# Kernel optimization log

Measured on AMD Instinct MI355X. Metric: run time of the kernel, lower is better.

## Reference

```python
import jax, jax.numpy as jnp
import numpy as np

N = 50000          # nodes
E = 800000         # edges (avg degree 16)
D_IN = 128
D_HID = 128
D_OUT = 64
NUM_GRAPHS = 64


def setup_inputs() -> dict:
    key = jax.random.key(0)
    ks = jax.random.split(key, 10)
    x = jax.random.normal(ks[0], (N, D_IN), dtype=jnp.float32)
    edge_index = jax.random.randint(ks[1], (2, E), 0, N, dtype=jnp.int64)
    batch = jnp.sort(jax.random.randint(ks[2], (N,), 0, NUM_GRAPHS, dtype=jnp.int64))
    def glorot(k, fan_in, fan_out):
        s = np.float32(np.sqrt(6.0 / (fan_in + fan_out)))
        return jax.random.uniform(k, (fan_in, fan_out), jnp.float32, -s, s)
    return {
        "x": x,
        "edge_index": edge_index,
        "batch": batch,
        "W1": glorot(ks[3], D_IN, D_HID),  "b1": jnp.zeros((D_HID,), jnp.float32),
        "W2": glorot(ks[4], D_HID, D_HID), "b2": jnp.zeros((D_HID,), jnp.float32),
        "W3": glorot(ks[5], D_HID, D_OUT), "b3": jnp.zeros((D_OUT,), jnp.float32),
    }


def _gcn_conv(x, W, b, src, dst, dis):
    # GCNConv: D^{-1/2}(A+I)D^{-1/2} X W + b  (self-loops handled analytically)
    h = x @ W                                   # [N, out]
    norm = dis[src] * dis[dst]                  # [E]
    agg = jax.ops.segment_sum(h[src] * norm[:, None], dst, num_segments=N)
    return agg + h * (dis * dis)[:, None] + b   # self-loop term + bias


def reference(x, edge_index, batch, W1, b1, W2, b2, W3, b3):
    src, dst = edge_index[0], edge_index[1]
    # degree with self-loop (matches PyG add_self_loops + gcn_norm)
    deg = jnp.zeros((N,), jnp.float32).at[dst].add(1.0) + 1.0
    dis = jax.lax.rsqrt(deg)                    # deg >= 1, no inf handling needed

    h = jax.nn.relu(_gcn_conv(x, W1, b1, src, dst, dis))
    h = jax.nn.relu(_gcn_conv(h, W2, b2, src, dst, dis))
    features = _gcn_conv(h, W3, b3, src, dst, dis)   # [N, D_OUT]

    sums = jax.ops.segment_sum(features, batch, num_segments=NUM_GRAPHS)
    cnts = jax.ops.segment_sum(jnp.ones((N,), jnp.float32), batch, num_segments=NUM_GRAPHS)
    avg_pool = sums / jnp.maximum(cnts, 1.0)[:, None]  # [NUM_GRAPHS, D_OUT]
    return features, avg_pool
```

## Files before the change

kernel.cpp:

```cpp
#include <hip/hip_runtime.h>


constexpr int KDIM = 128;
constexpr int NGRAPH = 64;

__device__ __forceinline__ unsigned bf16rne(float f) {
  unsigned u = __float_as_uint(f);
  return (u + 0x7fffu + ((u >> 16) & 1u)) >> 16;
}
__device__ __forceinline__ unsigned packbf2(float a, float b) {
  return bf16rne(a) | (bf16rne(b) << 16);
}
__device__ __forceinline__ float bflo(unsigned u) {
  return __uint_as_float(u << 16);
}
__device__ __forceinline__ float bfhi(unsigned u) {
  return __uint_as_float(u & 0xffff0000u);
}

__global__ void k_init(int* __restrict__ counts, int n) {
  int i = blockIdx.x * blockDim.x + threadIdx.x;
  int stride = gridDim.x * blockDim.x;
  for (int j = i; j < n; j += stride) counts[j] = 0;
}

__global__ void k_hist(const int* __restrict__ src, const int* __restrict__ dst,
                       int* __restrict__ counts, int e, int n) {
  int i = blockIdx.x * blockDim.x + threadIdx.x;
  int stride = gridDim.x * blockDim.x;
  for (int j = i; j < e; j += stride) {
    int s = src[j], d = dst[j];
    if ((unsigned)s < (unsigned)n && (unsigned)d < (unsigned)n)
      atomicAdd(&counts[d], 1);
  }
}

__global__ void k_dis(const int* __restrict__ counts, float* __restrict__ dis, int n) {
  int i = blockIdx.x * blockDim.x + threadIdx.x;
  int stride = gridDim.x * blockDim.x;
  for (int j = i; j < n; j += stride)
    dis[j] = rsqrtf((float)counts[j] + 1.0f);
}

__global__ void k_scan_block(const int* __restrict__ in, int* __restrict__ outExcl,
                             int* __restrict__ blockSums, int n) {
  __shared__ int s[256];
  int tid = threadIdx.x;
  int i = blockIdx.x * 256 + tid;
  int v = (i < n) ? in[i] : 0;
  int x = v;
  s[tid] = x;
  __syncthreads();
  for (int off = 1; off < 256; off <<= 1) {
    int t = (tid >= off) ? s[tid - off] : 0;
    __syncthreads();
    x += t;
    s[tid] = x;
    __syncthreads();
  }
  if (i < n) outExcl[i] = x - v;
  if (tid == 255) blockSums[blockIdx.x] = x;
}

__global__ void k_scan_offsets(int* __restrict__ bs, int nb) {
  __shared__ int s[256];
  int tid = threadIdx.x;
  int v = (tid < nb) ? bs[tid] : 0;
  int x = v;
  s[tid] = x;
  __syncthreads();
  for (int off = 1; off < 256; off <<= 1) {
    int t = (tid >= off) ? s[tid - off] : 0;
    __syncthreads();
    x += t;
    s[tid] = x;
    __syncthreads();
  }
  if (tid < nb) bs[tid] = x - v;
  if (tid == nb - 1) bs[256] = x;
}

__global__ void k_scan_add(int* __restrict__ row_start, const int* __restrict__ bs,
                           int* __restrict__ cursor, int n) {
  int i = blockIdx.x * blockDim.x + threadIdx.x;
  int stride = gridDim.x * blockDim.x;
  for (int j = i; j < n; j += stride) {
    int r = row_start[j] + bs[j >> 8];
    row_start[j] = r;
    cursor[j] = r;
  }
  if (i == 0) row_start[n] = bs[256];
}

__global__ void k_scatter(const int* __restrict__ src, const int* __restrict__ dst,
                          int* __restrict__ cursor, int* __restrict__ colA,
                          int e, int n) {
  int i = blockIdx.x * blockDim.x + threadIdx.x;
  int stride = gridDim.x * blockDim.x;
  for (int j = i; j < e; j += stride) {
    int s = src[j], d = dst[j];
    if ((unsigned)s < (unsigned)n && (unsigned)d < (unsigned)n) {
      int pos = atomicAdd(&cursor[d], 1);
      colA[pos] = s;
    }
  }
}

template <int DOUT>
__global__ __launch_bounds__(256) void k_gemm2b(const float* __restrict__ X,
                                                const float* __restrict__ W,
                                                unsigned short* __restrict__ Hb,
                                                int n) {
  __shared__ float xT[32][128];
  __shared__ float Wl[32][64];
  const int tid = threadIdx.x;
  const int tr = tid & 15;
  const int tc = tid >> 4;
  const int rowBase = blockIdx.x * 128;
  const int colBase = blockIdx.y * 64;

  float acc[8][4];
#pragma unroll
  for (int i = 0; i < 8; ++i)
#pragma unroll
    for (int j = 0; j < 4; ++j) acc[i][j] = 0.f;

  const int sr = tid >> 1;
  const int kh = (tid & 1) * 16;
  const int srow = min(rowBase + sr, n - 1);
  const float* xsrc = X + (size_t)srow * KDIM + kh;

  for (int k0 = 0; k0 < KDIM / 32; ++k0) {
    {
      const float4* s4 = reinterpret_cast<const float4*>(xsrc + k0 * 32);
      float4 v0 = s4[0], v1 = s4[1], v2 = s4[2], v3 = s4[3];
      xT[kh + 0][sr] = v0.x;  xT[kh + 1][sr] = v0.y;
      xT[kh + 2][sr] = v0.z;  xT[kh + 3][sr] = v0.w;
      xT[kh + 4][sr] = v1.x;  xT[kh + 5][sr] = v1.y;
      xT[kh + 6][sr] = v1.z;  xT[kh + 7][sr] = v1.w;
      xT[kh + 8][sr] = v2.x;  xT[kh + 9][sr] = v2.y;
      xT[kh + 10][sr] = v2.z; xT[kh + 11][sr] = v2.w;
      xT[kh + 12][sr] = v3.x; xT[kh + 13][sr] = v3.y;
      xT[kh + 14][sr] = v3.z; xT[kh + 15][sr] = v3.w;
    }
#pragma unroll
    for (int q = 0; q < 2; ++q) {
      int f4 = tid + q * 256;
      int k = f4 >> 4;
      int c4 = f4 & 15;
      *reinterpret_cast<float4*>(&Wl[k][c4 * 4]) = *reinterpret_cast<const float4*>(
          W + (size_t)(k0 * 32 + k) * DOUT + colBase + c4 * 4);
    }
    __syncthreads();
#pragma unroll 8
    for (int k = 0; k < 32; ++k) {
      float4 xa = *reinterpret_cast<const float4*>(&xT[k][tr * 4]);
      float4 xb = *reinterpret_cast<const float4*>(&xT[k][64 + tr * 4]);
      float4 wv = *reinterpret_cast<const float4*>(&Wl[k][tc * 4]);
      const float xs[8] = {xa.x, xa.y, xa.z, xa.w, xb.x, xb.y, xb.z, xb.w};
      const float ws[4] = {wv.x, wv.y, wv.z, wv.w};
#pragma unroll
      for (int i = 0; i < 8; ++i)
#pragma unroll
        for (int j = 0; j < 4; ++j) acc[i][j] = fmaf(xs[i], ws[j], acc[i][j]);
    }
    __syncthreads();
  }

#pragma unroll
  for (int i = 0; i < 8; ++i) {
    int row = rowBase + ((i < 4) ? (tr * 4 + i) : (64 + tr * 4 + i - 4));
    if (row < n) {
      uint2 o;
      o.x = packbf2(acc[i][0], acc[i][1]);
      o.y = packbf2(acc[i][2], acc[i][3]);
      *reinterpret_cast<uint2*>(Hb + (size_t)row * DOUT + colBase + tc * 4) = o;
    }
  }
}

template <int D, bool RELU>
__global__ __launch_bounds__(256, 4) void k_agg7(
    const unsigned short* __restrict__ Hb, const int* __restrict__ row_start,
    const int* __restrict__ colA, const float* __restrict__ dis,
    const float* __restrict__ bias, float* __restrict__ OUT, int n) {
  constexpr int C = D / 64;
  const int wave = threadIdx.x >> 6;
  const int lane = threadIdx.x & 63;
  const int nA = blockIdx.x * 8 + wave * 2;
  const int nB = nA + 1;
  const bool vA = nA < n, vB = nB < n;

  int eA = vA ? row_start[nA] : 0, endA = vA ? row_start[nA + 1] : 0;
  int eB = vB ? row_start[nB] : 0, endB = vB ? row_start[nB + 1] : 0;
  const float diA = vA ? dis[nA] : 0.f;
  const float diB = vB ? dis[nB] : 0.f;

  float aA0[C], aA1[C], aB0[C], aB1[C];
#pragma unroll
  for (int c = 0; c < C; ++c) { aA0[c] = 0.f; aA1[c] = 0.f; aB0[c] = 0.f; aB1[c] = 0.f; }

  auto hload = [&](int s) -> unsigned {
    if constexpr (C == 2)
      return reinterpret_cast<const unsigned*>(Hb + (size_t)s * D)[lane];
    else
      return (unsigned)Hb[(size_t)s * D + lane];
  };
  auto fma1 = [&](float* acc, unsigned u, float w) {
    acc[0] = fmaf(bflo(u), w, acc[0]);
    if constexpr (C == 2) acc[1] = fmaf(bfhi(u), w, acc[1]);
  };

  while (eA + 1 < endA && eB + 1 < endB) {
    const int sA0 = colA[eA], sA1 = colA[eA + 1];
    const int sB0 = colA[eB], sB1 = colA[eB + 1];
    const float wA0 = dis[sA0] * diA, wA1 = dis[sA1] * diA;
    const float wB0 = dis[sB0] * diB, wB1 = dis[sB1] * diB;
    const unsigned hA0 = hload(sA0), hA1 = hload(sA1);
    const unsigned hB0 = hload(sB0), hB1 = hload(sB1);
    fma1(aA0, hA0, wA0);
    fma1(aA1, hA1, wA1);
    fma1(aB0, hB0, wB0);
    fma1(aB1, hB1, wB1);
    eA += 2; eB += 2;
  }
  while (eA + 1 < endA) {
    const int s0 = colA[eA], s1 = colA[eA + 1];
    const float w0 = dis[s0] * diA, w1 = dis[s1] * diA;
    const unsigned h0 = hload(s0), h1 = hload(s1);
    fma1(aA0, h0, w0);
    fma1(aA1, h1, w1);
    eA += 2;
  }
  if (eA < endA) {
    const int s0 = colA[eA];
    fma1(aA0, hload(s0), dis[s0] * diA);
  }
  while (eB + 1 < endB) {
    const int s0 = colA[eB], s1 = colA[eB + 1];
    const float w0 = dis[s0] * diB, w1 = dis[s1] * diB;
    const unsigned h0 = hload(s0), h1 = hload(s1);
    fma1(aB0, h0, w0);
    fma1(aB1, h1, w1);
    eB += 2;
  }
  if (eB < endB) {
    const int s0 = colA[eB];
    fma1(aB0, hload(s0), dis[s0] * diB);
  }

  if (vA) {
    const unsigned u = hload(nA);
    const float di2 = diA * diA;
#pragma unroll
    for (int c = 0; c < C; ++c) {
      float h = (c == 0) ? bflo(u) : bfhi(u);
      float v = aA0[c] + aA1[c] + h * di2 + bias[C * lane + c];
      if (RELU) v = fmaxf(v, 0.f);
      OUT[(size_t)nA * D + C * lane + c] = v;
    }
  }
  if (vB) {
    const unsigned u = hload(nB);
    const float di2 = diB * diB;
#pragma unroll
    for (int c = 0; c < C; ++c) {
      float h = (c == 0) ? bflo(u) : bfhi(u);
      float v = aB0[c] + aB1[c] + h * di2 + bias[C * lane + c];
      if (RELU) v = fmaxf(v, 0.f);
      OUT[(size_t)nB * D + C * lane + c] = v;
    }
  }
}

__global__ __launch_bounds__(256) void k_pool2(const float* __restrict__ F,
                                               const int* __restrict__ batch,
                                               float* __restrict__ out, int n) {
  const int g = blockIdx.x;
  __shared__ int sb[2];
  if (threadIdx.x < 2) {
    int target = g + threadIdx.x;
    int lo = 0, hi = n;
    while (lo < hi) {
      int mid = (lo + hi) >> 1;
      if (batch[mid] < target) lo = mid + 1; else hi = mid;
    }
    sb[threadIdx.x] = lo;
  }
  __syncthreads();
  const int beg = sb[0], end = sb[1];
  const int wave = threadIdx.x >> 6;
  const int lane = threadIdx.x & 63;
  float acc = 0.f;
  for (int node = beg + wave; node < end; node += 4)
    acc += F[(size_t)node * 64 + lane];
  __shared__ float red[4][64];
  red[wave][lane] = acc;
  __syncthreads();
  if (wave == 0) {
    float v = (red[0][lane] + red[1][lane]) + (red[2][lane] + red[3][lane]);
    out[g * 64 + lane] = v / fmaxf((float)(end - beg), 1.f);
  }
}

extern "C" void kernel_launch(void* const* d_in, const int* in_sizes, int n_in,
                              void* d_out, int out_size, void* d_ws, size_t ws_size,
                              hipStream_t stream) {
  const float* x     = (const float*)d_in[0];
  const int*   ei    = (const int*)d_in[1];
  const int*   batch = (const int*)d_in[2];
  const float* W1 = (const float*)d_in[3];
  const float* b1 = (const float*)d_in[4];
  const float* W2 = (const float*)d_in[5];
  const float* b2 = (const float*)d_in[6];
  const float* W3 = (const float*)d_in[7];
  const float* b3 = (const float*)d_in[8];

  const int n = in_sizes[0] / KDIM;
  const int e = in_sizes[1] / 2;
  const int* src = ei;
  const int* dst = ei + e;

  char* p = (char*)d_ws;
  size_t off = 0;
  auto carve = [&](size_t bytes) {
    char* r = p + off;
    off = (off + bytes + 255) & ~(size_t)255;
    return r;
  };
  unsigned short* Hb = (unsigned short*)carve((size_t)n * KDIM * 2);
  float* F           = (float*)carve((size_t)n * KDIM * 4);
  float* dis         = (float*)carve((size_t)n * 4);
  int*   counts      = (int*)carve((size_t)n * 4);
  int*   row_start   = (int*)carve((size_t)(n + 1) * 4);
  int*   cursor      = (int*)carve((size_t)n * 4);
  int*   colA        = (int*)carve((size_t)e * 4);
  int*   blockSums   = (int*)carve(512 * 4);
  (void)ws_size;

  const int nb1 = (n + 255) / 256;
  const int GS = 1024;

  k_init<<<GS, 256, 0, stream>>>(counts, n);
  k_hist<<<GS, 256, 0, stream>>>(src, dst, counts, e, n);
  k_dis<<<nb1, 256, 0, stream>>>(counts, dis, n);
  k_scan_block<<<nb1, 256, 0, stream>>>(counts, row_start, blockSums, n);
  k_scan_offsets<<<1, 256, 0, stream>>>(blockSums, nb1);
  k_scan_add<<<nb1, 256, 0, stream>>>(row_start, blockSums, cursor, n);
  k_scatter<<<GS, 256, 0, stream>>>(src, dst, cursor, colA, e, n);

  const int rowBlocks = (n + 127) / 128;
  const int aggGrid = (n + 7) / 8;

  k_gemm2b<128><<<dim3(rowBlocks, 2), 256, 0, stream>>>(x, W1, Hb, n);
  k_agg7<128, true><<<aggGrid, 256, 0, stream>>>(Hb, row_start, colA, dis, b1, F, n);
  k_gemm2b<128><<<dim3(rowBlocks, 2), 256, 0, stream>>>(F, W2, Hb, n);
  k_agg7<128, true><<<aggGrid, 256, 0, stream>>>(Hb, row_start, colA, dis, b2, F, n);
  k_gemm2b<64><<<dim3(rowBlocks, 1), 256, 0, stream>>>(F, W3, Hb, n);
  k_agg7<64, false><<<aggGrid, 256, 0, stream>>>(Hb, row_start, colA, dis, b3,
                                                 (float*)d_out, n);
  k_pool2<<<NGRAPH, 256, 0, stream>>>((const float*)d_out, batch,
                                      (float*)d_out + (size_t)n * 64, n);
}
```

Before: 446.3 us.

## Partition histogram and CSR scatter atomics by destination range across block groups

The degree histogram and CSR scatter kernels now split destination nodes into 8 contiguous ranges. Each block is assigned one range by its block index (blockIdx.x & 7), scans the full edge list, and does atomics only for edges whose destination falls in that range. The aim is to keep each block group's atomic targets inside a smaller address window, presumably one that fits better in the cache partitions of MI355X, to cut atomic contention and cache thrashing. The cost is that dst is read 8 times in total across the groups, src is still read once per edge, and the degree check no longer looks at src validity, so it now differs slightly from the scatter.

```diff
diff --git a/kernel.cpp b/kernel.cpp
--- a/kernel.cpp
+++ b/kernel.cpp
@@ -3,6 +3,7 @@
 
 constexpr int KDIM = 128;
 constexpr int NGRAPH = 64;
+constexpr int NPART = 8;
 
 __device__ __forceinline__ unsigned bf16rne(float f) {
   unsigned u = __float_as_uint(f);
@@ -24,14 +25,18 @@
   for (int j = i; j < n; j += stride) counts[j] = 0;
 }
 
-__global__ void k_hist(const int* __restrict__ src, const int* __restrict__ dst,
-                       int* __restrict__ counts, int e, int n) {
-  int i = blockIdx.x * blockDim.x + threadIdx.x;
-  int stride = gridDim.x * blockDim.x;
+__global__ void k_hist_p(const int* __restrict__ dst, int* __restrict__ counts,
+                         int e, int n, int chunk) {
+  const int p = blockIdx.x & (NPART - 1);
+  const int inst = blockIdx.x >> 3;
+  const int nInst = gridDim.x >> 3;
+  const int lo = p * chunk;
+  const int hi = min(n, lo + chunk);
+  int i = inst * blockDim.x + threadIdx.x;
+  const int stride = nInst * blockDim.x;
   for (int j = i; j < e; j += stride) {
-    int s = src[j], d = dst[j];
-    if ((unsigned)s < (unsigned)n && (unsigned)d < (unsigned)n)
-      atomicAdd(&counts[d], 1);
+    const int d = dst[j];
+    if (d >= lo && d < hi) atomicAdd(&counts[d], 1);
   }
 }
 
@@ -92,16 +97,24 @@
   if (i == 0) row_start[n] = bs[256];
 }
 
-__global__ void k_scatter(const int* __restrict__ src, const int* __restrict__ dst,
-                          int* __restrict__ cursor, int* __restrict__ colA,
-                          int e, int n) {
-  int i = blockIdx.x * blockDim.x + threadIdx.x;
-  int stride = gridDim.x * blockDim.x;
+__global__ void k_scatter_p(const int* __restrict__ src, const int* __restrict__ dst,
+                            int* __restrict__ cursor, int* __restrict__ colA,
+                            int e, int n, int chunk) {
+  const int p = blockIdx.x & (NPART - 1);
+  const int inst = blockIdx.x >> 3;
+  const int nInst = gridDim.x >> 3;
+  const int lo = p * chunk;
+  const int hi = min(n, lo + chunk);
+  int i = inst * blockDim.x + threadIdx.x;
+  const int stride = nInst * blockDim.x;
   for (int j = i; j < e; j += stride) {
-    int s = src[j], d = dst[j];
-    if ((unsigned)s < (unsigned)n && (unsigned)d < (unsigned)n) {
-      int pos = atomicAdd(&cursor[d], 1);
-      colA[pos] = s;
+    const int d = dst[j];
+    if (d >= lo && d < hi) {
+      const int s = src[j];
+      if ((unsigned)s < (unsigned)n) {
+        int pos = atomicAdd(&cursor[d], 1);
+        colA[pos] = s;
+      }
     }
   }
 }
@@ -339,15 +352,15 @@
   (void)ws_size;
 
   const int nb1 = (n + 255) / 256;
-  const int GS = 1024;
-
-  k_init<<<GS, 256, 0, stream>>>(counts, n);
-  k_hist<<<GS, 256, 0, stream>>>(src, dst, counts, e, n);
+  const int chunk = (n + NPART - 1) / NPART;
+
+  k_init<<<512, 256, 0, stream>>>(counts, n);
+  k_hist_p<<<1024, 256, 0, stream>>>(dst, counts, e, n, chunk);
   k_dis<<<nb1, 256, 0, stream>>>(counts, dis, n);
   k_scan_block<<<nb1, 256, 0, stream>>>(counts, row_start, blockSums, n);
   k_scan_offsets<<<1, 256, 0, stream>>>(blockSums, nb1);
   k_scan_add<<<nb1, 256, 0, stream>>>(row_start, blockSums, cursor, n);
-  k_scatter<<<GS, 256, 0, stream>>>(src, dst, cursor, colA, e, n);
+  k_scatter_p<<<1024, 256, 0, stream>>>(src, dst, cursor, colA, e, n, chunk);
 
   const int rowBlocks = (n + 127) / 128;
   const int aggGrid = (n + 7) / 8;
```

Result: faster. 425.8 us (-4.6%).
